# Kernel tuning notes

Measured on AMD Instinct MI355X. Metric: run time of the kernel, lower is better.

The kernel has to match this reference:

```python
import jax, jax.numpy as jnp
import numpy as np

B, L, D = 32, 4096, 1024


def setup_inputs() -> dict:
    key = jax.random.key(0)
    k_h, k_idx, k_w1, k_w2 = jax.random.split(key, 4)
    h = jax.random.normal(k_h, (B, L, D), dtype=jnp.float32)
    # 4 sorted positions per sample: [s1, e1, s2, e2]; +arange*2 guarantees
    # strict increase and a non-empty context region (s2 > e1 + 1).
    raw = jnp.sort(jax.random.randint(k_idx, (B, 4), 0, L - 10), axis=-1)
    pts = raw + jnp.arange(4, dtype=raw.dtype) * 2
    span1_idx = pts[:, 0:2].reshape(B, 1, 2).astype(jnp.int64)
    span2_idx = pts[:, 2:4].reshape(B, 1, 2).astype(jnp.int64)
    scale1 = 1.0 / np.sqrt(3 * D)
    scale2 = 1.0 / np.sqrt(D)
    W1 = jax.random.normal(k_w1, (3 * D, D), dtype=jnp.float32) * scale1
    b1 = jnp.zeros((D,), dtype=jnp.float32)
    W2 = jax.random.normal(k_w2, (D, D), dtype=jnp.float32) * scale2
    b2 = jnp.zeros((D,), dtype=jnp.float32)
    return {"h": h, "span1_idx": span1_idx, "span2_idx": span2_idx,
            "W1": W1, "b1": b1, "W2": W2, "b2": b2}


def _masked_mean(h, lo, hi_excl):
    # mean of h[b, lo[b]:hi_excl[b], :] over the length axis, vectorized
    pos = jnp.arange(h.shape[1])  # [L]
    mask = ((pos[None, :] >= lo[:, None]) & (pos[None, :] < hi_excl[:, None])).astype(h.dtype)  # [B,L]
    cnt = jnp.maximum(mask.sum(axis=1, keepdims=True), 1.0)  # [B,1]
    return jnp.einsum('bl,bld->bd', mask, h) / cnt  # [B,D]


def reference(h, span1_idx, span2_idx, W1, b1, W2, b2):
    s1, e1 = span1_idx[:, 0, 0], span1_idx[:, 0, 1]
    s2, e2 = span2_idx[:, 0, 0], span2_idx[:, 0, 1]
    span1_rep = _masked_mean(h, s1, e1 + 1)          # span tokens inclusive
    span2_rep = _masked_mean(h, s2, e2 + 1)
    context_rep = _masked_mean(h, e1 + 1, s2)        # tokens strictly between spans
    combined = jnp.concatenate([span1_rep, context_rep, span2_rep], axis=-1)  # [B,3D]
    hmid = jax.nn.relu(combined @ W1 + b1)
    out = hmid @ W2 + b2
    return out[:, None, :]  # [B,1,D]
```

## Files before the change

### kernel.cpp

```cpp
#include <hip/hip_runtime.h>

#define BB 32
#define LL 4096
#define DD 1024
#define CH 16
#define G1 1024
#define K2_TILE 64
#define K3_TILE 32

static __device__ __forceinline__ int imax(int a, int b) { return a > b ? a : b; }
static __device__ __forceinline__ int imin(int a, int b) { return a < b ? a : b; }

__global__ __launch_bounds__(256) void k0_zero(float* __restrict__ ws,
                                               float* __restrict__ out) {
    const int i = blockIdx.x * 256 + threadIdx.x;
    const float4 z = make_float4(0.f, 0.f, 0.f, 0.f);
    if (i < 32768) ((float4*)ws)[i] = z;
    else ((float4*)out)[i - 32768] = z;
}

static __device__ __forceinline__ void accum_rows_add(const float* __restrict__ hb,
                                                      int beg, int end, float4& acc) {
    float4 a0 = make_float4(0.f, 0.f, 0.f, 0.f);
    float4 a1 = make_float4(0.f, 0.f, 0.f, 0.f);
    float4 a2 = make_float4(0.f, 0.f, 0.f, 0.f);
    float4 a3 = make_float4(0.f, 0.f, 0.f, 0.f);
    int l = beg;
    for (; l + 4 <= end; l += 4) {
        float4 v0 = *(const float4*)(hb + (size_t)(l + 0) * DD);
        float4 v1 = *(const float4*)(hb + (size_t)(l + 1) * DD);
        float4 v2 = *(const float4*)(hb + (size_t)(l + 2) * DD);
        float4 v3 = *(const float4*)(hb + (size_t)(l + 3) * DD);
        a0.x += v0.x; a0.y += v0.y; a0.z += v0.z; a0.w += v0.w;
        a1.x += v1.x; a1.y += v1.y; a1.z += v1.z; a1.w += v1.w;
        a2.x += v2.x; a2.y += v2.y; a2.z += v2.z; a2.w += v2.w;
        a3.x += v3.x; a3.y += v3.y; a3.z += v3.z; a3.w += v3.w;
    }
    for (; l < end; ++l) {
        float4 v = *(const float4*)(hb + (size_t)l * DD);
        a0.x += v.x; a0.y += v.y; a0.z += v.z; a0.w += v.w;
    }
    acc.x += (a0.x + a1.x) + (a2.x + a3.x);
    acc.y += (a0.y + a1.y) + (a2.y + a3.y);
    acc.z += (a0.z + a1.z) + (a2.z + a3.z);
    acc.w += (a0.w + a1.w) + (a2.w + a3.w);
}

__global__ __launch_bounds__(256) void k1_sums(const float* __restrict__ h,
                                               const int* __restrict__ sp1,
                                               const int* __restrict__ sp2,
                                               float* __restrict__ sums) {
    const int tid = threadIdx.x;

    int NC = 0;
#pragma unroll
    for (int b = 0; b < BB; ++b) {
        const int len = sp2[2 * b + 1] - sp1[2 * b] + 1;
        NC += (len + CH - 1) / CH;
    }
    const int q = (NC + (int)gridDim.x - 1) / (int)gridDim.x;
    const int c0 = blockIdx.x * q;
    const int c1 = imin(c0 + q, NC);
    if (c0 >= c1) return;

    int b = 0, base = 0, s1, e1, s2, e2, ncb;
    for (;; ++b) {
        s1 = sp1[2 * b]; e1 = sp1[2 * b + 1];
        s2 = sp2[2 * b]; e2 = sp2[2 * b + 1];
        ncb = (e2 - s1 + 1 + CH - 1) / CH;
        if (c0 < base + ncb) break;
        base += ncb;
    }
    const float* hb = h + (size_t)b * LL * DD + (size_t)tid * 4;
    float* dstb = sums + (size_t)b * 3 * DD + (size_t)tid * 4;

    float* kdst = nullptr;
    float4 acc = make_float4(0.f, 0.f, 0.f, 0.f);
    for (int c = c0; c < c1; ++c) {
        if (c >= base + ncb) {
            base += ncb; ++b;
            s1 = sp1[2 * b]; e1 = sp1[2 * b + 1];
            s2 = sp2[2 * b]; e2 = sp2[2 * b + 1];
            ncb = (e2 - s1 + 1 + CH - 1) / CH;
            hb = h + (size_t)b * LL * DD + (size_t)tid * 4;
            dstb = sums + (size_t)b * 3 * DD + (size_t)tid * 4;
        }
        const int beg = s1 + (c - base) * CH;
        const int end = imin(beg + CH, e2 + 1);
        const int lo[3] = {beg, imax(beg, e1 + 1), imax(beg, s2)};
        const int hi[3] = {imin(end, e1 + 1), imin(end, s2), end};
#pragma unroll
        for (int sgi = 0; sgi < 3; ++sgi) {
            if (lo[sgi] < hi[sgi]) {
                float* d = dstb + sgi * DD;
                if (d != kdst) {
                    if (kdst) {
                        atomicAdd(kdst + 0, acc.x); atomicAdd(kdst + 1, acc.y);
                        atomicAdd(kdst + 2, acc.z); atomicAdd(kdst + 3, acc.w);
                    }
                    kdst = d;
                    acc = make_float4(0.f, 0.f, 0.f, 0.f);
                }
                accum_rows_add(hb, lo[sgi], hi[sgi], acc);
            }
        }
    }
    if (kdst) {
        atomicAdd(kdst + 0, acc.x); atomicAdd(kdst + 1, acc.y);
        atomicAdd(kdst + 2, acc.z); atomicAdd(kdst + 3, acc.w);
    }
}

__global__ __launch_bounds__(256) void k2_gemm1(const float* __restrict__ sums,
                                                const int* __restrict__ sp1,
                                                const int* __restrict__ sp2,
                                                const float* __restrict__ W1,
                                                float* __restrict__ hmid) {
    __shared__ float cl[K2_TILE * BB];
    __shared__ float icl[BB];
    const int tid = threadIdx.x;
    const int j = blockIdx.x * 256 + tid;
    const int k0 = blockIdx.y * K2_TILE;
    const int seg = k0 / DD;

    if (tid < BB) {
        const int b = tid;
        const int s1 = sp1[2 * b], e1 = sp1[2 * b + 1];
        const int s2 = sp2[2 * b], e2 = sp2[2 * b + 1];
        const int cnt = (seg == 0) ? (e1 + 1 - s1) : (seg == 1) ? (s2 - e1 - 1) : (e2 + 1 - s2);
        icl[b] = 1.0f / (float)imax(cnt, 1);
    }
    __syncthreads();
    for (int i = tid; i < K2_TILE * BB; i += 256) {
        const int kk = i / BB;
        const int b = i % BB;
        cl[i] = sums[(size_t)b * (3 * DD) + (k0 + kk)] * icl[b];
    }
    __syncthreads();

    float acc[BB];
#pragma unroll
    for (int b = 0; b < BB; ++b) acc[b] = 0.f;

    const float* w = W1 + (size_t)k0 * DD + j;
    for (int kk = 0; kk < K2_TILE; ++kk) {
        const float wv = w[(size_t)kk * DD];
        const float4* c4 = (const float4*)(cl + kk * BB);
#pragma unroll
        for (int qq = 0; qq < BB / 4; ++qq) {
            float4 c = c4[qq];
            acc[4 * qq + 0] = fmaf(c.x, wv, acc[4 * qq + 0]);
            acc[4 * qq + 1] = fmaf(c.y, wv, acc[4 * qq + 1]);
            acc[4 * qq + 2] = fmaf(c.z, wv, acc[4 * qq + 2]);
            acc[4 * qq + 3] = fmaf(c.w, wv, acc[4 * qq + 3]);
        }
    }
#pragma unroll
    for (int b = 0; b < BB; ++b) atomicAdd(&hmid[(size_t)b * DD + j], acc[b]);
}

__global__ __launch_bounds__(256) void k3_gemm2(const float* __restrict__ hmid,
                                                const float* __restrict__ b1,
                                                const float* __restrict__ W2,
                                                const float* __restrict__ b2,
                                                float* __restrict__ out) {
    __shared__ float al[K3_TILE * BB];
    const int tid = threadIdx.x;
    const int j = blockIdx.x * 256 + tid;
    const int k0 = blockIdx.y * K3_TILE;

    for (int i = tid; i < K3_TILE * BB; i += 256) {
        const int kk = i / BB;
        const int b = i % BB;
        const float v = hmid[(size_t)b * DD + (k0 + kk)] + b1[k0 + kk];
        al[i] = fmaxf(v, 0.f);
    }
    __syncthreads();

    float acc[BB];
    const float bias = (blockIdx.y == 0) ? b2[j] : 0.f;
#pragma unroll
    for (int b = 0; b < BB; ++b) acc[b] = bias;

    const float* w = W2 + (size_t)k0 * DD + j;
    for (int kk = 0; kk < K3_TILE; ++kk) {
        const float wv = w[(size_t)kk * DD];
        const float4* c4 = (const float4*)(al + kk * BB);
#pragma unroll
        for (int qq = 0; qq < BB / 4; ++qq) {
            float4 c = c4[qq];
            acc[4 * qq + 0] = fmaf(c.x, wv, acc[4 * qq + 0]);
            acc[4 * qq + 1] = fmaf(c.y, wv, acc[4 * qq + 1]);
            acc[4 * qq + 2] = fmaf(c.z, wv, acc[4 * qq + 2]);
            acc[4 * qq + 3] = fmaf(c.w, wv, acc[4 * qq + 3]);
        }
    }
#pragma unroll
    for (int b = 0; b < BB; ++b) atomicAdd(&out[(size_t)b * DD + j], acc[b]);
}

extern "C" void kernel_launch(void* const* d_in, const int* in_sizes, int n_in,
                              void* d_out, int out_size, void* d_ws, size_t ws_size,
                              hipStream_t stream) {
    const float* h = (const float*)d_in[0];
    const int* sp1 = (const int*)d_in[1];
    const int* sp2 = (const int*)d_in[2];
    const float* W1 = (const float*)d_in[3];
    const float* b1 = (const float*)d_in[4];
    const float* W2 = (const float*)d_in[5];
    const float* b2 = (const float*)d_in[6];
    float* out = (float*)d_out;

    float* sums = (float*)d_ws;
    float* hmid = sums + BB * 3 * DD;

    k0_zero<<<160, 256, 0, stream>>>((float*)d_ws, out);
    k1_sums<<<G1, 256, 0, stream>>>(h, sp1, sp2, sums);
    k2_gemm1<<<dim3(DD / 256, 3 * DD / K2_TILE), 256, 0, stream>>>(sums, sp1, sp2, W1, hmid);
    k3_gemm2<<<dim3(DD / 256, DD / K3_TILE), 256, 0, stream>>>(hmid, b1, W2, b2, out);
}
```

Baseline: 111.2 us.

## Replace atomic span-sum accumulation with per-block partial slots and a reduction kernel

Measured after the change: 139.8 us. +25.7%, slower.

```diff
diff --git a/kernel.cpp b/kernel.cpp
--- a/kernel.cpp
+++ b/kernel.cpp
@@ -4,19 +4,20 @@
 #define LL 4096
 #define DD 1024
 #define CH 16
-#define G1 1024
+#define G1 2048
+#define SLOTS 12
 #define K2_TILE 64
 #define K3_TILE 32
 
 static __device__ __forceinline__ int imax(int a, int b) { return a > b ? a : b; }
 static __device__ __forceinline__ int imin(int a, int b) { return a < b ? a : b; }
 
-__global__ __launch_bounds__(256) void k0_zero(float* __restrict__ ws,
+__global__ __launch_bounds__(256) void k0_zero(float* __restrict__ hmid,
                                                float* __restrict__ out) {
     const int i = blockIdx.x * 256 + threadIdx.x;
     const float4 z = make_float4(0.f, 0.f, 0.f, 0.f);
-    if (i < 32768) ((float4*)ws)[i] = z;
-    else ((float4*)out)[i - 32768] = z;
+    if (i < 8192) ((float4*)hmid)[i] = z;
+    else ((float4*)out)[i - 8192] = z;
 }
 
 static __device__ __forceinline__ void accum_rows_add(const float* __restrict__ hb,
@@ -49,7 +50,7 @@
 __global__ __launch_bounds__(256) void k1_sums(const float* __restrict__ h,
                                                const int* __restrict__ sp1,
                                                const int* __restrict__ sp2,
-                                               float* __restrict__ sums) {
+                                               float* __restrict__ part) {
     const int tid = threadIdx.x;
 
     int NC = 0;
@@ -58,7 +59,7 @@
         const int len = sp2[2 * b + 1] - sp1[2 * b] + 1;
         NC += (len + CH - 1) / CH;
     }
-    const int q = (NC + (int)gridDim.x - 1) / (int)gridDim.x;
+    const int q = (NC + G1 - 1) / G1;
     const int c0 = blockIdx.x * q;
     const int c1 = imin(c0 + q, NC);
     if (c0 >= c1) return;
@@ -71,10 +72,11 @@
         if (c0 < base + ncb) break;
         base += ncb;
     }
+    const int bfirst = b;
     const float* hb = h + (size_t)b * LL * DD + (size_t)tid * 4;
-    float* dstb = sums + (size_t)b * 3 * DD + (size_t)tid * 4;
-
-    float* kdst = nullptr;
+    float* slot0 = part + (size_t)blockIdx.x * SLOTS * DD + (size_t)tid * 4;
+
+    int kcur = -1;
     float4 acc = make_float4(0.f, 0.f, 0.f, 0.f);
     for (int c = c0; c < c1; ++c) {
         if (c >= base + ncb) {
@@ -83,32 +85,111 @@
             s2 = sp2[2 * b]; e2 = sp2[2 * b + 1];
             ncb = (e2 - s1 + 1 + CH - 1) / CH;
             hb = h + (size_t)b * LL * DD + (size_t)tid * 4;
-            dstb = sums + (size_t)b * 3 * DD + (size_t)tid * 4;
-        }
+        }
+        const int jloc = b - bfirst;
         const int beg = s1 + (c - base) * CH;
         const int end = imin(beg + CH, e2 + 1);
         const int lo[3] = {beg, imax(beg, e1 + 1), imax(beg, s2)};
         const int hi[3] = {imin(end, e1 + 1), imin(end, s2), end};
 #pragma unroll
-        for (int sgi = 0; sgi < 3; ++sgi) {
-            if (lo[sgi] < hi[sgi]) {
-                float* d = dstb + sgi * DD;
-                if (d != kdst) {
-                    if (kdst) {
-                        atomicAdd(kdst + 0, acc.x); atomicAdd(kdst + 1, acc.y);
-                        atomicAdd(kdst + 2, acc.z); atomicAdd(kdst + 3, acc.w);
-                    }
-                    kdst = d;
+        for (int s = 0; s < 3; ++s) {
+            if (lo[s] < hi[s]) {
+                const int key = jloc * 3 + s;
+                if (key != kcur) {
+                    if (kcur >= 0) *(float4*)(slot0 + (size_t)kcur * DD) = acc;
+                    kcur = key;
                     acc = make_float4(0.f, 0.f, 0.f, 0.f);
                 }
-                accum_rows_add(hb, lo[sgi], hi[sgi], acc);
+                accum_rows_add(hb, lo[s], hi[s], acc);
             }
         }
     }
-    if (kdst) {
-        atomicAdd(kdst + 0, acc.x); atomicAdd(kdst + 1, acc.y);
-        atomicAdd(kdst + 2, acc.z); atomicAdd(kdst + 3, acc.w);
-    }
+    if (kcur >= 0) *(float4*)(slot0 + (size_t)kcur * DD) = acc;
+}
+
+__global__ __launch_bounds__(256) void k1c_reduce(const float* __restrict__ part,
+                                                  const int* __restrict__ sp1,
+                                                  const int* __restrict__ sp2,
+                                                  float* __restrict__ sums) {
+    const int key = blockIdx.x;
+    const int b = key / 3, s = key % 3;
+    const int tid = threadIdx.x;
+
+    int NC = 0, base_b = 0;
+    for (int bb = 0; bb < BB; ++bb) {
+        const int len = sp2[2 * bb + 1] - sp1[2 * bb] + 1;
+        const int nc = (len + CH - 1) / CH;
+        if (bb < b) base_b += nc;
+        NC += nc;
+    }
+    const int s1 = sp1[2 * b], e1 = sp1[2 * b + 1];
+    const int s2 = sp2[2 * b], e2 = sp2[2 * b + 1];
+    const int ncb = (e2 - s1 + 1 + CH - 1) / CH;
+    const int q = (NC + G1 - 1) / G1;
+    const int lo_s = (s == 0) ? s1 : (s == 1) ? e1 + 1 : s2;
+    const int hi_s = (s == 0) ? e1 + 1 : (s == 1) ? s2 : e2 + 1;
+
+    const int bk_lo = base_b / q;
+    const int bk_hi = (base_b + ncb - 1) / q;
+
+    int bb = 0, bbase = 0;
+    {
+        const int c = bk_lo * q;
+        for (;;) {
+            const int len = sp2[2 * bb + 1] - sp1[2 * bb] + 1;
+            const int nc = (len + CH - 1) / CH;
+            if (c < bbase + nc) break;
+            bbase += nc; ++bb;
+        }
+    }
+
+    float4 a0 = make_float4(0.f, 0.f, 0.f, 0.f);
+    float4 a1 = a0, a2 = a0, a3 = a0;
+    const float4 z = a0;
+
+    for (int bk = bk_lo; bk <= bk_hi; bk += 4) {
+        const float* p0 = nullptr; const float* p1 = nullptr;
+        const float* p2 = nullptr; const float* p3 = nullptr;
+#pragma unroll
+        for (int u = 0; u < 4; ++u) {
+            const int bkk = bk + u;
+            if (bkk > bk_hi) break;
+            const int cc0 = bkk * q;
+            const int cc1 = imin(cc0 + q, NC);
+            for (;;) {
+                const int len = sp2[2 * bb + 1] - sp1[2 * bb] + 1;
+                const int nc = (len + CH - 1) / CH;
+                if (cc0 < bbase + nc) break;
+                bbase += nc; ++bb;
+            }
+            const int clo = imax(cc0, base_b);
+            const int chi = imin(cc1, base_b + ncb);
+            if (clo >= chi) continue;
+            const int rbeg = s1 + (clo - base_b) * CH;
+            const int rend = imin(s1 + (chi - base_b) * CH, e2 + 1);
+            const int beg = imax(rbeg, lo_s);
+            const int end = imin(rend, hi_s);
+            if (beg < end) {
+                const int slot = (b - bb) * 3 + s;
+                const float* p = part + ((size_t)bkk * SLOTS + slot) * DD + (size_t)tid * 4;
+                if (u == 0) p0 = p; else if (u == 1) p1 = p; else if (u == 2) p2 = p; else p3 = p;
+            }
+        }
+        const float4 v0 = p0 ? *(const float4*)p0 : z;
+        const float4 v1 = p1 ? *(const float4*)p1 : z;
+        const float4 v2 = p2 ? *(const float4*)p2 : z;
+        const float4 v3 = p3 ? *(const float4*)p3 : z;
+        a0.x += v0.x; a0.y += v0.y; a0.z += v0.z; a0.w += v0.w;
+        a1.x += v1.x; a1.y += v1.y; a1.z += v1.z; a1.w += v1.w;
+        a2.x += v2.x; a2.y += v2.y; a2.z += v2.z; a2.w += v2.w;
+        a3.x += v3.x; a3.y += v3.y; a3.z += v3.z; a3.w += v3.w;
+    }
+    float4 r;
+    r.x = (a0.x + a1.x) + (a2.x + a3.x);
+    r.y = (a0.y + a1.y) + (a2.y + a3.y);
+    r.z = (a0.z + a1.z) + (a2.z + a3.z);
+    r.w = (a0.w + a1.w) + (a2.w + a3.w);
+    *(float4*)(sums + ((size_t)b * 3 + s) * DD + (size_t)tid * 4) = r;
 }
 
 __global__ __launch_bounds__(256) void k2_gemm1(const float* __restrict__ sums,
@@ -213,9 +294,11 @@
 
     float* sums = (float*)d_ws;
     float* hmid = sums + BB * 3 * DD;
-
-    k0_zero<<<160, 256, 0, stream>>>((float*)d_ws, out);
-    k1_sums<<<G1, 256, 0, stream>>>(h, sp1, sp2, sums);
+    float* part = hmid + BB * DD;
+
+    k0_zero<<<64, 256, 0, stream>>>(hmid, out);
+    k1_sums<<<G1, 256, 0, stream>>>(h, sp1, sp2, part);
+    k1c_reduce<<<96, 256, 0, stream>>>(part, sp1, sp2, sums);
     k2_gemm1<<<dim3(DD / 256, 3 * DD / K2_TILE), 256, 0, stream>>>(sums, sp1, sp2, W1, hmid);
     k3_gemm2<<<dim3(DD / 256, DD / K3_TILE), 256, 0, stream>>>(hmid, b1, W2, b2, out);
 }
```

## Replace GEMM atomics with partial buffers plus reduce kernels; rebalance sum grid

Applied to the files above, without the earlier changes.

Result: slower. 125.4 us (+12.7%).

```diff
diff --git a/kernel.cpp b/kernel.cpp
--- a/kernel.cpp
+++ b/kernel.cpp
@@ -4,19 +4,17 @@
 #define LL 4096
 #define DD 1024
 #define CH 16
-#define G1 1024
+#define G1 2048
 #define K2_TILE 64
 #define K3_TILE 32
+#define NY2 (3 * DD / K2_TILE)
+#define NY3 (DD / K3_TILE)
 
 static __device__ __forceinline__ int imax(int a, int b) { return a > b ? a : b; }
 static __device__ __forceinline__ int imin(int a, int b) { return a < b ? a : b; }
 
-__global__ __launch_bounds__(256) void k0_zero(float* __restrict__ ws,
-                                               float* __restrict__ out) {
-    const int i = blockIdx.x * 256 + threadIdx.x;
-    const float4 z = make_float4(0.f, 0.f, 0.f, 0.f);
-    if (i < 32768) ((float4*)ws)[i] = z;
-    else ((float4*)out)[i - 32768] = z;
+__global__ __launch_bounds__(256) void k0_zero(float* __restrict__ sums) {
+    ((float4*)sums)[blockIdx.x * 256 + threadIdx.x] = make_float4(0.f, 0.f, 0.f, 0.f);
 }
 
 static __device__ __forceinline__ void accum_rows_add(const float* __restrict__ hb,
@@ -58,9 +56,10 @@
         const int len = sp2[2 * b + 1] - sp1[2 * b] + 1;
         NC += (len + CH - 1) / CH;
     }
-    const int q = (NC + (int)gridDim.x - 1) / (int)gridDim.x;
-    const int c0 = blockIdx.x * q;
-    const int c1 = imin(c0 + q, NC);
+    const int q = NC / G1, r = NC % G1;
+    const int bk = blockIdx.x;
+    const int c0 = bk * q + imin(bk, r);
+    const int c1 = c0 + q + (bk < r ? 1 : 0);
     if (c0 >= c1) return;
 
     int b = 0, base = 0, s1, e1, s2, e2, ncb;
@@ -90,9 +89,9 @@
         const int lo[3] = {beg, imax(beg, e1 + 1), imax(beg, s2)};
         const int hi[3] = {imin(end, e1 + 1), imin(end, s2), end};
 #pragma unroll
-        for (int sgi = 0; sgi < 3; ++sgi) {
-            if (lo[sgi] < hi[sgi]) {
-                float* d = dstb + sgi * DD;
+        for (int s = 0; s < 3; ++s) {
+            if (lo[s] < hi[s]) {
+                float* d = dstb + s * DD;
                 if (d != kdst) {
                     if (kdst) {
                         atomicAdd(kdst + 0, acc.x); atomicAdd(kdst + 1, acc.y);
@@ -101,7 +100,7 @@
                     kdst = d;
                     acc = make_float4(0.f, 0.f, 0.f, 0.f);
                 }
-                accum_rows_add(hb, lo[sgi], hi[sgi], acc);
+                accum_rows_add(hb, lo[s], hi[s], acc);
             }
         }
     }
@@ -115,7 +114,7 @@
                                                 const int* __restrict__ sp1,
                                                 const int* __restrict__ sp2,
                                                 const float* __restrict__ W1,
-                                                float* __restrict__ hmid) {
+                                                float* __restrict__ part2) {
     __shared__ float cl[K2_TILE * BB];
     __shared__ float icl[BB];
     const int tid = threadIdx.x;
@@ -143,6 +142,7 @@
     for (int b = 0; b < BB; ++b) acc[b] = 0.f;
 
     const float* w = W1 + (size_t)k0 * DD + j;
+#pragma unroll 4
     for (int kk = 0; kk < K2_TILE; ++kk) {
         const float wv = w[(size_t)kk * DD];
         const float4* c4 = (const float4*)(cl + kk * BB);
@@ -155,15 +155,31 @@
             acc[4 * qq + 3] = fmaf(c.w, wv, acc[4 * qq + 3]);
         }
     }
-#pragma unroll
-    for (int b = 0; b < BB; ++b) atomicAdd(&hmid[(size_t)b * DD + j], acc[b]);
+    float* p = part2 + ((size_t)blockIdx.y * BB) * DD + j;
+#pragma unroll
+    for (int b = 0; b < BB; ++b) p[(size_t)b * DD] = acc[b];
+}
+
+__global__ __launch_bounds__(256) void k2b_reduce(const float* __restrict__ part2,
+                                                  const float* __restrict__ b1,
+                                                  float* __restrict__ hmid) {
+    const int j = blockIdx.x * 256 + threadIdx.x;
+    const int b = blockIdx.y;
+    const float* p = part2 + (size_t)b * DD + j;
+    float s0 = 0.f, s1 = 0.f, s2 = 0.f, s3 = 0.f;
+#pragma unroll
+    for (int y = 0; y < NY2; y += 4) {
+        s0 += p[(size_t)(y + 0) * BB * DD];
+        s1 += p[(size_t)(y + 1) * BB * DD];
+        s2 += p[(size_t)(y + 2) * BB * DD];
+        s3 += p[(size_t)(y + 3) * BB * DD];
+    }
+    hmid[(size_t)b * DD + j] = fmaxf((s0 + s1) + (s2 + s3) + b1[j], 0.f);
 }
 
 __global__ __launch_bounds__(256) void k3_gemm2(const float* __restrict__ hmid,
-                                                const float* __restrict__ b1,
                                                 const float* __restrict__ W2,
-                                                const float* __restrict__ b2,
-                                                float* __restrict__ out) {
+                                                float* __restrict__ part3) {
     __shared__ float al[K3_TILE * BB];
     const int tid = threadIdx.x;
     const int j = blockIdx.x * 256 + tid;
@@ -172,17 +188,16 @@
     for (int i = tid; i < K3_TILE * BB; i += 256) {
         const int kk = i / BB;
         const int b = i % BB;
-        const float v = hmid[(size_t)b * DD + (k0 + kk)] + b1[k0 + kk];
-        al[i] = fmaxf(v, 0.f);
+        al[i] = hmid[(size_t)b * DD + (k0 + kk)];
     }
     __syncthreads();
 
     float acc[BB];
-    const float bias = (blockIdx.y == 0) ? b2[j] : 0.f;
-#pragma unroll
-    for (int b = 0; b < BB; ++b) acc[b] = bias;
+#pragma unroll
+    for (int b = 0; b < BB; ++b) acc[b] = 0.f;
 
     const float* w = W2 + (size_t)k0 * DD + j;
+#pragma unroll 4
     for (int kk = 0; kk < K3_TILE; ++kk) {
         const float wv = w[(size_t)kk * DD];
         const float4* c4 = (const float4*)(al + kk * BB);
@@ -195,8 +210,26 @@
             acc[4 * qq + 3] = fmaf(c.w, wv, acc[4 * qq + 3]);
         }
     }
-#pragma unroll
-    for (int b = 0; b < BB; ++b) atomicAdd(&out[(size_t)b * DD + j], acc[b]);
+    float* p = part3 + ((size_t)blockIdx.y * BB) * DD + j;
+#pragma unroll
+    for (int b = 0; b < BB; ++b) p[(size_t)b * DD] = acc[b];
+}
+
+__global__ __launch_bounds__(256) void k3b_reduce(const float* __restrict__ part3,
+                                                  const float* __restrict__ b2,
+                                                  float* __restrict__ out) {
+    const int j = blockIdx.x * 256 + threadIdx.x;
+    const int b = blockIdx.y;
+    const float* p = part3 + (size_t)b * DD + j;
+    float s0 = 0.f, s1 = 0.f, s2 = 0.f, s3 = 0.f;
+#pragma unroll
+    for (int y = 0; y < NY3; y += 4) {
+        s0 += p[(size_t)(y + 0) * BB * DD];
+        s1 += p[(size_t)(y + 1) * BB * DD];
+        s2 += p[(size_t)(y + 2) * BB * DD];
+        s3 += p[(size_t)(y + 3) * BB * DD];
+    }
+    out[(size_t)b * DD + j] = (s0 + s1) + (s2 + s3) + b2[j];
 }
 
 extern "C" void kernel_launch(void* const* d_in, const int* in_sizes, int n_in,
@@ -213,9 +246,13 @@
 
     float* sums = (float*)d_ws;
     float* hmid = sums + BB * 3 * DD;
-
-    k0_zero<<<160, 256, 0, stream>>>((float*)d_ws, out);
+    float* part2 = hmid + BB * DD;
+    float* part3 = part2 + (size_t)NY2 * BB * DD;
+
+    k0_zero<<<96, 256, 0, stream>>>(sums);
     k1_sums<<<G1, 256, 0, stream>>>(h, sp1, sp2, sums);
-    k2_gemm1<<<dim3(DD / 256, 3 * DD / K2_TILE), 256, 0, stream>>>(sums, sp1, sp2, W1, hmid);
-    k3_gemm2<<<dim3(DD / 256, DD / K3_TILE), 256, 0, stream>>>(hmid, b1, W2, b2, out);
-}
+    k2_gemm1<<<dim3(DD / 256, NY2), 256, 0, stream>>>(sums, sp1, sp2, W1, part2);
+    k2b_reduce<<<dim3(DD / 256, BB), 256, 0, stream>>>(part2, b1, hmid);
+    k3_gemm2<<<dim3(DD / 256, NY3), 256, 0, stream>>>(hmid, W2, part3);
+    k3b_reduce<<<dim3(DD / 256, BB), 256, 0, stream>>>(part3, b2, out);
+}
```
